# Kernel tuning notes

Hardware: AMD Instinct MI355X
Metric: run time of the kernel (lower is better)

Reference implementation:

```python
import jax, jax.numpy as jnp
import numpy as np

GRAPH_ALPHA = 3.0
HOP_ALPHA = 0.05
TOP_K = 30


def conv1x1(x, W, b):
    # x: [B,C,N,T], W: [O,C] -> [B,O,N,T]
    return jnp.einsum('bcnt,oc->bont', x, W) + b[None, :, None, None]


def tconv(x, W, b):
    # temporal conv along T, kernel (1,3), 'same' padding. W: [O,I,1,3]
    y = jax.lax.conv_general_dilated(x, W, (1, 1), ((0, 0), (1, 1)),
                                     dimension_numbers=('NCHW', 'OIHW', 'NCHW'))
    return y + b[None, :, None, None]


def mixprop(x, adj, W, b):
    # 1-hop mix-prop graph diffusion (gcn_depth=1, hopalpha=0.05)
    n = adj.shape[0]
    A = adj + jnp.eye(n, dtype=adj.dtype)
    A = A / A.sum(axis=1, keepdims=True)
    h = HOP_ALPHA * x + (1.0 - HOP_ALPHA) * jnp.einsum('bcvt,vw->bcwt', x, A)
    return conv1x1(jnp.concatenate([x, h], axis=1), W, b)


def st_block(x, adj, tf_w, tf_b, tg_w, tg_b, g1_w, g1_b, g2_w, g2_b,
             end_w, end_b, out_w, out_b):
    h = jnp.tanh(tconv(x, tf_w, tf_b)) * jax.nn.sigmoid(tconv(x, tg_w, tg_b))
    h = mixprop(h, adj, g1_w, g1_b) + mixprop(h, adj.T, g2_w, g2_b)
    h = jax.nn.relu(conv1x1(h, end_w, end_b))
    return conv1x1(h, out_w, out_b)


def build_adj(idx, emb1, emb2, l1_w, l1_b, l2_w, l2_b):
    e1, e2 = emb1[idx], emb2[idx]
    n1 = jnp.tanh(GRAPH_ALPHA * (e1 @ l1_w.T + l1_b))
    n2 = jnp.tanh(GRAPH_ALPHA * (e2 @ l2_w.T + l2_b))
    a = n1 @ n2.T - n2 @ n1.T
    adj = jax.nn.relu(jnp.tanh(GRAPH_ALPHA * a))
    _, top_idx = jax.lax.top_k(adj, TOP_K)
    rows = jnp.arange(adj.shape[0])[:, None]
    mask = jnp.zeros_like(adj).at[rows, top_idx].set(1.0)
    return adj * mask


def setup_inputs() -> dict:
    B, T, N, D = 16, 128, 1024, 64
    ks = jax.random.split(jax.random.key(0), 24)
    def w(i, shape):
        return jax.random.normal(ks[i], shape, dtype=jnp.float32) * 0.1
    z = lambda *s: jnp.zeros(s, jnp.float32)
    return {
        'x': jax.random.normal(ks[0], (B, T, N), dtype=jnp.float32),
        'idx': jnp.arange(N, dtype=jnp.int32),
        'emb1': w(1, (N, D)), 'emb2': w(2, (N, D)),
        'lin1_w': w(3, (D, D)), 'lin1_b': z(D),
        'lin2_w': w(4, (D, D)), 'lin2_b': z(D),
        'w_start': w(5, (16, 1)), 'b_start': z(16),
        'enc_tf_w': w(6, (16, 16, 1, 3)), 'enc_tf_b': z(16),
        'enc_tg_w': w(7, (16, 16, 1, 3)), 'enc_tg_b': z(16),
        'enc_g1_w': w(8, (16, 32)), 'enc_g1_b': z(16),
        'enc_g2_w': w(9, (16, 32)), 'enc_g2_b': z(16),
        'enc_end_w': w(10, (32, 16)), 'enc_end_b': z(32),
        'enc_out_w': w(11, (64, 32)), 'enc_out_b': z(64),
        'dec_tf_w': w(12, (64, 64, 1, 3)), 'dec_tf_b': z(64),
        'dec_tg_w': w(13, (64, 64, 1, 3)), 'dec_tg_b': z(64),
        'dec_g1_w': w(14, (64, 128)), 'dec_g1_b': z(64),
        'dec_g2_w': w(15, (64, 128)), 'dec_g2_b': z(64),
        'dec_end_w': w(16, (32, 64)), 'dec_end_b': z(32),
        'dec_out_w': w(17, (16, 32)), 'dec_out_b': z(16),
        'w_end': w(18, (1, 16)), 'b_end': z(1),
    }


def reference(x, idx, emb1, emb2, lin1_w, lin1_b, lin2_w, lin2_b,
              w_start, b_start,
              enc_tf_w, enc_tf_b, enc_tg_w, enc_tg_b, enc_g1_w, enc_g1_b,
              enc_g2_w, enc_g2_b, enc_end_w, enc_end_b, enc_out_w, enc_out_b,
              dec_tf_w, dec_tf_b, dec_tg_w, dec_tg_b, dec_g1_w, dec_g1_b,
              dec_g2_w, dec_g2_b, dec_end_w, dec_end_b, dec_out_w, dec_out_b,
              w_end, b_end):
    adj = build_adj(idx, emb1, emb2, lin1_w, lin1_b, lin2_w, lin2_b)
    h = jnp.transpose(x, (0, 2, 1))[:, None]  # [B,1,N,T]
    h = conv1x1(h, w_start, b_start)          # [B,16,N,T]
    z = st_block(h, adj, enc_tf_w, enc_tf_b, enc_tg_w, enc_tg_b,
                 enc_g1_w, enc_g1_b, enc_g2_w, enc_g2_b,
                 enc_end_w, enc_end_b, enc_out_w, enc_out_b)  # [B,64,N,T]
    y = st_block(z, adj, dec_tf_w, dec_tf_b, dec_tg_w, dec_tg_b,
                 dec_g1_w, dec_g1_b, dec_g2_w, dec_g2_b,
                 dec_end_w, dec_end_b, dec_out_w, dec_out_b)  # [B,16,N,T]
    y = conv1x1(y, w_end, b_end)               # [B,1,N,T]
    return jnp.transpose(y[:, 0], (0, 2, 1))   # [B,T,N]
```

## Files before the change

kernel.cpp:

```cpp
#include <hip/hip_runtime.h>
#include <math.h>

#define NN   1024
#define TTL  128
#define NTP  131072
#define TOPK 30

#define OEGTF_T 0
#define OEGTF_C 48
#define OEGTF_B 96
#define OEGTG_T 112
#define OEGTG_C 160
#define OEGTG_B 208
#define OEE0    224
#define OEE1    736
#define OEE2    1248
#define OEEB    1760
#define OEOUT_W 1792
#define OEOUT_B 3840
#define ODTF_B  16192
#define ODTG_B  28544
#define ODEB    34752
#define OWC     34784
#define OBC     34816
#define ODEALL  59456
#define ODTW2   65600
#define OCF     77888
#define OCG     78080
#define WTOT    78272


__global__ void k_prep_weights(
    const float* __restrict__ w_start, const float* __restrict__ b_start,
    const float* __restrict__ etf_w, const float* __restrict__ etf_b,
    const float* __restrict__ etg_w, const float* __restrict__ etg_b,
    const float* __restrict__ eg1_w, const float* __restrict__ eg1_b,
    const float* __restrict__ eg2_w, const float* __restrict__ eg2_b,
    const float* __restrict__ eend_w, const float* __restrict__ eend_b,
    const float* __restrict__ eout_w, const float* __restrict__ eout_b,
    const float* __restrict__ dtf_w, const float* __restrict__ dtf_b,
    const float* __restrict__ dtg_w, const float* __restrict__ dtg_b,
    const float* __restrict__ dg1_w, const float* __restrict__ dg1_b,
    const float* __restrict__ dg2_w, const float* __restrict__ dg2_b,
    const float* __restrict__ dend_w, const float* __restrict__ dend_b,
    const float* __restrict__ dout_w, const float* __restrict__ dout_b,
    const float* __restrict__ w_end, const float* __restrict__ b_end,
    float* __restrict__ W)
{
    int tid = blockIdx.x*blockDim.x + threadIdx.x;
    int nthr = gridDim.x*blockDim.x;
    for (int id=tid; id<96; id+=nthr){
        int which = id/48; int r = id%48; int o = r/3, k = r%3;
        const float* w = which ? etg_w : etf_w;
        double t=0.0, c=0.0;
        for (int i=0;i<16;i++){
            double wv = (double)w[(o*16+i)*3+k];
            t += wv*(double)w_start[i];
            c += wv*(double)b_start[i];
        }
        W[(which?OEGTG_T:OEGTF_T)+o*3+k] = (float)t;
        W[(which?OEGTG_C:OEGTF_C)+o*3+k] = (float)c;
    }
    for (int i=tid;i<16;i+=nthr){
        W[OEGTF_B+i] = etf_b[i];
        W[OEGTG_B+i] = etg_b[i];
    }
    for (int id=tid; id<512; id+=nthr){
        int i = id>>5, o2 = id&31;
        double s0=0.0, s1=0.0, s2=0.0;
        for (int o=0;o<16;o++){
            double m0 = (double)eg1_w[o*32+i] + (double)eg2_w[o*32+i]
                      + 0.05*((double)eg1_w[o*32+16+i] + (double)eg2_w[o*32+16+i]);
            double m1 = 0.95*(double)eg1_w[o*32+16+i];
            double m2 = 0.95*(double)eg2_w[o*32+16+i];
            double ew = (double)eend_w[o2*16+o];
            s0 += ew*m0; s1 += ew*m1; s2 += ew*m2;
        }
        W[OEE0+i*32+o2]=(float)s0; W[OEE1+i*32+o2]=(float)s1; W[OEE2+i*32+o2]=(float)s2;
    }
    for (int o2=tid; o2<32; o2+=nthr){
        double s = (double)eend_b[o2];
        for (int o=0;o<16;o++) s += (double)eend_w[o2*16+o]*((double)eg1_b[o]+(double)eg2_b[o]);
        W[OEEB+o2] = (float)s;
    }
    for (int i=tid;i<64;i+=nthr){
        W[ODTF_B+i]=dtf_b[i]; W[ODTG_B+i]=dtg_b[i];
    }
    for (int id=tid; id<12288; id+=nthr){
        int oc = id/3072; int rem = id%3072; int j = rem/96; int q = rem%96;
        const float* w = (q<48) ? dtf_w : dtg_w;
        int q2 = (q<48) ? q : q-48;
        int o = q2/3, k = q2%3;
        double s = 0.0;
        for (int i=0;i<64;i++)
            s += (double)w[((oc*16+o)*64+i)*3+k]*(double)eout_w[i*32+j];
        W[ODTW2+id] = (float)s;
    }
    for (int id=tid; id<384; id+=nthr){
        int which = id/192; int r = id%192;
        int oc = r/48; int q = r%48; int o = q/3, k = q%3;
        const float* w = which ? dtg_w : dtf_w;
        double s = 0.0;
        for (int i=0;i<64;i++)
            s += (double)w[((oc*16+o)*64+i)*3+k]*(double)eout_b[i];
        W[(which?OCG:OCF) + oc*48 + o*3 + k] = (float)s;
    }
    for (int id=tid; id<6144; id+=nthr){
        int i = id/96, j = id%96;
        double s = 0.0;
        if (j < 32){
            int o2 = j;
            for (int o=0;o<64;o++){
                double m1 = 0.95*(double)dg1_w[o*128+64+i];
                s += (double)dend_w[o2*64+o]*m1;
            }
        } else if (j < 64){
            int o2 = j-32;
            for (int o=0;o<64;o++){
                double m2 = 0.95*(double)dg2_w[o*128+64+i];
                s += (double)dend_w[o2*64+o]*m2;
            }
        } else {
            int o2 = j-64;
            for (int o=0;o<64;o++){
                double m0 = (double)dg1_w[o*128+i] + (double)dg2_w[o*128+i]
                          + 0.05*((double)dg1_w[o*128+64+i] + (double)dg2_w[o*128+64+i]);
                s += (double)dend_w[o2*64+o]*m0;
            }
        }
        W[ODEALL+id] = (float)s;
    }
    for (int o2=tid; o2<32; o2+=nthr){
        double s = (double)dend_b[o2];
        for (int o=0;o<64;o++) s += (double)dend_w[o2*64+o]*((double)dg1_b[o]+(double)dg2_b[o]);
        W[ODEB+o2] = (float)s;
        double wc = 0.0;
        for (int o3=0;o3<16;o3++) wc += (double)w_end[o3]*(double)dout_w[o3*32+o2];
        W[OWC+o2] = (float)wc;
    }
    if (tid==0){
        double bc = (double)b_end[0];
        for (int o3=0;o3<16;o3++) bc += (double)w_end[o3]*(double)dout_b[o3];
        W[OBC] = (float)bc;
    }
}

__global__ void k_emb(const int* __restrict__ idxp,
                      const float* __restrict__ emb1, const float* __restrict__ emb2,
                      const float* __restrict__ l1w, const float* __restrict__ l1b,
                      const float* __restrict__ l2w, const float* __restrict__ l2b,
                      double* __restrict__ n1, double* __restrict__ n2)
{
    int id = blockIdx.x*blockDim.x + threadIdx.x;
    int i = id>>6, d = id&63;
    int ii = idxp[i];
    double a1 = (double)l1b[d], a2 = (double)l2b[d];
    for (int k=0;k<64;k++){
        a1 += (double)emb1[ii*64+k]*(double)l1w[d*64+k];
        a2 += (double)emb2[ii*64+k]*(double)l2w[d*64+k];
    }
    n1[id] = tanh(3.0*a1);
    n2[id] = tanh(3.0*a2);
}

__global__ __launch_bounds__(64) void k_topk(
    const double* __restrict__ n1, const double* __restrict__ n2,
    int* __restrict__ topc, double* __restrict__ topv,
    double* __restrict__ rs1, double* __restrict__ colsum)
{
    __shared__ double arow[NN];
    __shared__ double sn1[64], sn2[64];
    int i = blockIdx.x, lane = threadIdx.x;
    sn1[lane] = n1[i*64+lane];
    sn2[lane] = n2[i*64+lane];
    __syncthreads();
    for (int jb=0;jb<16;jb++){
        int j = jb*64 + lane;
        const double* p2 = n2 + j*64;
        const double* p1 = n1 + j*64;
        double d1v=0.0, d2v=0.0;
        for (int d=0;d<64;d++){ d1v += sn1[d]*p2[d]; d2v += sn2[d]*p1[d]; }
        double a = tanh(3.0*(d1v - d2v));
        arow[j] = a>0.0 ? a : 0.0;
    }
    __syncthreads();
    double rsum = 0.0;
    for (int r=0;r<TOPK;r++){
        double bv = -2.0; int bj = 1<<30;
        for (int jb=0;jb<16;jb++){
            int j = jb*64+lane;
            double v = arow[j];
            if (v>bv || (v==bv && j<bj)){ bv=v; bj=j; }
        }
        for (int off=32; off>=1; off>>=1){
            double ov = __shfl_xor(bv, off, 64);
            int    oj = __shfl_xor(bj, off, 64);
            if (ov>bv || (ov==bv && oj<bj)){ bv=ov; bj=oj; }
        }
        if (lane == (bj & 63)) arow[bj] = -2.0;
        if (lane == 0){
            topc[i*TOPK+r] = bj;
            topv[i*TOPK+r] = bv;
            if (bv > 0.0) atomicAdd(&colsum[bj], bv);
        }
        rsum += (bv > 0.0 ? bv : 0.0);
        __syncthreads();
    }
    if (lane == 0) rs1[i] = 1.0 + rsum;
}

__global__ void k_csc(const int* __restrict__ topc, const double* __restrict__ topv,
                      const double* __restrict__ rs1,
                      int* __restrict__ ccount, int* __restrict__ cidx, float* __restrict__ cw)
{
    int w = blockIdx.x*blockDim.x + threadIdx.x;
    if (w >= NN) return;
    double rv = rs1[w];
    for (int r=0;r<TOPK;r++){
        double v = topv[w*TOPK+r];
        if (v > 0.0){
            int col = topc[w*TOPK+r];
            int pos = atomicAdd(&ccount[col], 1);
            cidx[(long)col*NN+pos] = w;
            cw  [(long)col*NN+pos] = (float)(v / rv);
        }
    }
}

__global__ void k_pad(int* __restrict__ ccount, int* __restrict__ cidx, float* __restrict__ cw)
{
    int col = blockIdx.x*blockDim.x + threadIdx.x;
    if (col >= NN) return;
    int cnt = ccount[col];
    int padded = (cnt + 7) & ~7;
    for (int e = cnt; e < padded; e++){
        cidx[(long)col*NN + e] = 0;
        cw  [(long)col*NN + e] = 0.0f;
    }
    ccount[col] = padded;
}

__global__ void k_post1(const double* __restrict__ colsum, const double* __restrict__ rs1,
                        double* __restrict__ rs2, float* __restrict__ d1, float* __restrict__ d2)
{
    int v = blockIdx.x*blockDim.x + threadIdx.x;
    if (v >= NN) return;
    double r2 = 1.0 + colsum[v];
    rs2[v] = r2;
    d2[v] = (float)(1.0/r2);
    d1[v] = (float)(1.0/rs1[v]);
}

__global__ void k_post2(const int* __restrict__ topc, const double* __restrict__ topv,
                        const double* __restrict__ rs2,
                        int* __restrict__ topc2, float* __restrict__ ew2b)
{
    int e = blockIdx.x*blockDim.x + threadIdx.x;
    if (e >= NN*32) return;
    int w = e>>5, r = e&31;
    if (r < TOPK){
        double v = topv[w*TOPK+r];
        int c = topc[w*TOPK+r];
        topc2[e] = (v > 0.0) ? c : 0;
        ew2b[e]  = (v > 0.0) ? (float)(v / rs2[c]) : 0.0f;
    } else {
        topc2[e] = 0;
        ew2b[e]  = 0.0f;
    }
}


__global__ __launch_bounds__(256) void k_enc_gg(const float* __restrict__ x,
    float* __restrict__ eg, float* __restrict__ es1, float* __restrict__ es2,
    const float* __restrict__ Wt,
    const int* __restrict__ ccount, const int* __restrict__ cidx, const float* __restrict__ cw,
    const int* __restrict__ topc2, const float* __restrict__ ew2b,
    const float* __restrict__ d1, const float* __restrict__ d2,
    long S, int b0)
{
    __shared__ float4 lds4[NN];
    int tid = threadIdx.x, c = blockIdx.y, cb = blockIdx.z, t0 = blockIdx.x*4;
    float ft[3], fc[3], gt[3], gcc[3];
    #pragma unroll
    for (int k=0;k<3;k++){
        ft[k]=Wt[OEGTF_T+c*3+k]; fc[k]=Wt[OEGTF_C+c*3+k];
        gt[k]=Wt[OEGTG_T+c*3+k]; gcc[k]=Wt[OEGTG_C+c*3+k];
    }
    float fb = Wt[OEGTF_B+c], gb = Wt[OEGTG_B+c];
    const float* xb = x + (long)(b0+cb)*NTP + (long)t0*NN;
    long base = (long)c*S + (long)cb*NTP + (long)t0*NN;
    bool hl0 = (t0>0), hr3 = (t0+4<TTL);
    for (int q=0;q<4;q++){
        int v = q*256 + tid;
        float xm = hl0 ? xb[v-NN] : 0.0f;
        float x0 = xb[v], x1 = xb[v+NN], x2 = xb[v+2*NN], x3 = xb[v+3*NN];
        float xq = hr3 ? xb[v+4*NN] : 0.0f;
        float g0,g1,g2,g3;
        {
            float atf = fb + ft[1]*x0 + fc[1], atg = gb + gt[1]*x0 + gcc[1];
            if (hl0){ atf += ft[0]*xm + fc[0]; atg += gt[0]*xm + gcc[0]; }
            atf += ft[2]*x1 + fc[2]; atg += gt[2]*x1 + gcc[2];
            g0 = tanhf(atf)/(1.0f+expf(-atg));
        }
        {
            float atf = fb + ft[0]*x0 + fc[0] + ft[1]*x1 + fc[1] + ft[2]*x2 + fc[2];
            float atg = gb + gt[0]*x0 + gcc[0] + gt[1]*x1 + gcc[1] + gt[2]*x2 + gcc[2];
            g1 = tanhf(atf)/(1.0f+expf(-atg));
        }
        {
            float atf = fb + ft[0]*x1 + fc[0] + ft[1]*x2 + fc[1] + ft[2]*x3 + fc[2];
            float atg = gb + gt[0]*x1 + gcc[0] + gt[1]*x2 + gcc[1] + gt[2]*x3 + gcc[2];
            g2 = tanhf(atf)/(1.0f+expf(-atg));
        }
        {
            float atf = fb + ft[0]*x2 + fc[0] + ft[1]*x3 + fc[1];
            float atg = gb + gt[0]*x2 + gcc[0] + gt[1]*x3 + gcc[1];
            if (hr3){ atf += ft[2]*xq + fc[2]; atg += gt[2]*xq + gcc[2]; }
            g3 = tanhf(atf)/(1.0f+expf(-atg));
        }
        lds4[v] = make_float4(g0,g1,g2,g3);
        eg[base+v] = g0; eg[base+NN+v] = g1; eg[base+2*NN+v] = g2; eg[base+3*NN+v] = g3;
    }
    __syncthreads();
    for (int wb=0;wb<4;wb++){
        int w = wb*256 + tid;
        float4 gw = lds4[w];
        float dv = d1[w];
        float a0=gw.x*dv, a1=gw.y*dv, a2=gw.z*dv, a3=gw.w*dv;
        int cnt = ccount[w];
        const int4*   ci4 = (const int4*)  (cidx + (long)w*NN);
        const float4* cw4 = (const float4*)(cw   + (long)w*NN);
        for (int e=0; e<cnt; e+=8){
            int4 ia = ci4[e>>2], ib = ci4[(e>>2)+1];
            float4 wa = cw4[e>>2], wc = cw4[(e>>2)+1];
            float4 s;
            s = lds4[ia.x]; a0 += wa.x*s.x; a1 += wa.x*s.y; a2 += wa.x*s.z; a3 += wa.x*s.w;
            s = lds4[ia.y]; a0 += wa.y*s.x; a1 += wa.y*s.y; a2 += wa.y*s.z; a3 += wa.y*s.w;
            s = lds4[ia.z]; a0 += wa.z*s.x; a1 += wa.z*s.y; a2 += wa.z*s.z; a3 += wa.z*s.w;
            s = lds4[ia.w]; a0 += wa.w*s.x; a1 += wa.w*s.y; a2 += wa.w*s.z; a3 += wa.w*s.w;
            s = lds4[ib.x]; a0 += wc.x*s.x; a1 += wc.x*s.y; a2 += wc.x*s.z; a3 += wc.x*s.w;
            s = lds4[ib.y]; a0 += wc.y*s.x; a1 += wc.y*s.y; a2 += wc.y*s.z; a3 += wc.y*s.w;
            s = lds4[ib.z]; a0 += wc.z*s.x; a1 += wc.z*s.y; a2 += wc.z*s.z; a3 += wc.z*s.w;
            s = lds4[ib.w]; a0 += wc.w*s.x; a1 += wc.w*s.y; a2 += wc.w*s.z; a3 += wc.w*s.w;
        }
        es1[base+w]=a0; es1[base+NN+w]=a1; es1[base+2*NN+w]=a2; es1[base+3*NN+w]=a3;
        float dw = d2[w];
        float b0a=gw.x*dw, b1a=gw.y*dw, b2a=gw.z*dw, b3a=gw.w*dw;
        const int4*   tc4 = (const int4*)  (topc2 + w*32);
        const float4* e24 = (const float4*)(ew2b  + w*32);
        #pragma unroll
        for (int r=0;r<8;r++){
            int4 ic = tc4[r]; float4 wv = e24[r];
            float4 s;
            s = lds4[ic.x]; b0a += wv.x*s.x; b1a += wv.x*s.y; b2a += wv.x*s.z; b3a += wv.x*s.w;
            s = lds4[ic.y]; b0a += wv.y*s.x; b1a += wv.y*s.y; b2a += wv.y*s.z; b3a += wv.y*s.w;
            s = lds4[ic.z]; b0a += wv.z*s.x; b1a += wv.z*s.y; b2a += wv.z*s.z; b3a += wv.z*s.w;
            s = lds4[ic.w]; b0a += wv.w*s.x; b1a += wv.w*s.y; b2a += wv.w*s.z; b3a += wv.w*s.w;
        }
        es2[base+w]=b0a; es2[base+NN+w]=b1a; es2[base+2*NN+w]=b2a; es2[base+3*NN+w]=b3a;
    }
}

__global__ __launch_bounds__(256) void k_enc_tail(const float* __restrict__ Bp,
    float* __restrict__ E32, const float* __restrict__ Wt, long S)
{
    long p = (long)blockIdx.x*256 + threadIdx.x;
    float e[32];
    #pragma unroll
    for (int o2=0;o2<32;o2++) e[o2] = Wt[OEEB+o2];
    for (int i=0;i<16;i++){
        float a = Bp[(long)i*S+p], b = Bp[(long)(16+i)*S+p], c = Bp[(long)(32+i)*S+p];
        const float* w0 = Wt+OEE0+i*32;
        const float* w1 = Wt+OEE1+i*32;
        const float* w2 = Wt+OEE2+i*32;
        #pragma unroll
        for (int o2=0;o2<32;o2++) e[o2] += w0[o2]*a + w1[o2]*b + w2[o2]*c;
    }
    #pragma unroll
    for (int o2=0;o2<32;o2++){
        float v = e[o2];
        E32[(long)o2*S+p] = v>0.0f ? v : 0.0f;
    }
}

__global__ __launch_bounds__(256) void k_dec_gate(const float* __restrict__ E32,
    float* __restrict__ g, const float* __restrict__ Wt, long S)
{
    int oc = blockIdx.y;
    long pos = (long)blockIdx.x*256 + threadIdx.x;
    int t = (int)((pos>>10) & (TTL-1));
    bool hasL = (t>0), hasR = (t<TTL-1);
    float af[16], ag[16];
    #pragma unroll
    for (int o=0;o<16;o++){
        float bf = Wt[ODTF_B+oc*16+o] + Wt[OCF+oc*48+o*3+1];
        float bg = Wt[ODTG_B+oc*16+o] + Wt[OCG+oc*48+o*3+1];
        if (hasL){ bf += Wt[OCF+oc*48+o*3];   bg += Wt[OCG+oc*48+o*3]; }
        if (hasR){ bf += Wt[OCF+oc*48+o*3+2]; bg += Wt[OCG+oc*48+o*3+2]; }
        af[o]=bf; ag[o]=bg;
    }
    #pragma unroll 1
    for (int j=0;j<32;j++){
        const float* xp = E32 + (long)j*S + pos;
        float xc = xp[0];
        float xl = hasL ? xp[-NN] : 0.0f;
        float xr = hasR ? xp[NN]  : 0.0f;
        const float* wfg = Wt + ODTW2 + (long)(oc*32+j)*96;
        #pragma unroll
        for (int o=0;o<16;o++){
            af[o] += wfg[o*3]*xl + wfg[o*3+1]*xc + wfg[o*3+2]*xr;
            ag[o] += wfg[48+o*3]*xl + wfg[48+o*3+1]*xc + wfg[48+o*3+2]*xr;
        }
    }
    #pragma unroll
    for (int o=0;o<16;o++){
        g[(long)(oc*16+o)*S + pos] = tanhf(af[o])/(1.0f+expf(-ag[o]));
    }
}

__global__ __launch_bounds__(256) void k_dec_conv(const float* __restrict__ g,
    float* __restrict__ Cp, float* __restrict__ P0p,
    const float* __restrict__ Wt, long S)
{
    long p = (long)blockIdx.x*256 + threadIdx.x;
    int jc = blockIdx.y;
    if (jc == 0){
        float a1[32], a2[32];
        #pragma unroll
        for (int jj=0;jj<32;jj++){ a1[jj]=0.0f; a2[jj]=0.0f; }
        #pragma unroll 1
        for (int i=0;i<64;i++){
            float gv = g[(long)i*S+p];
            const float* wr = Wt + ODEALL + i*96;
            #pragma unroll
            for (int jj=0;jj<32;jj++){ a1[jj] += wr[jj]*gv; a2[jj] += wr[32+jj]*gv; }
        }
        #pragma unroll
        for (int jj=0;jj<32;jj++){
            Cp[(long)jj*S+p] = a1[jj];
            Cp[(long)(32+jj)*S+p] = a2[jj];
        }
    } else {
        float a0[32];
        #pragma unroll
        for (int jj=0;jj<32;jj++) a0[jj] = Wt[ODEB+jj];
        #pragma unroll 1
        for (int i=0;i<64;i++){
            float gv = g[(long)i*S+p];
            const float* wr = Wt + ODEALL + i*96 + 64;
            #pragma unroll
            for (int jj=0;jj<32;jj++) a0[jj] += wr[jj]*gv;
        }
        #pragma unroll
        for (int jj=0;jj<32;jj++) P0p[(long)jj*S+p] = a0[jj];
    }
}

__global__ __launch_bounds__(256) void k_graph32(const float* __restrict__ P1,
    const float* __restrict__ P2, float* __restrict__ Q12,
    const int* __restrict__ ccount, const int* __restrict__ cidx, const float* __restrict__ cw,
    const int* __restrict__ topc2, const float* __restrict__ ew2b,
    const float* __restrict__ d1, const float* __restrict__ d2, long S)
{
    __shared__ float4 lds4[2*NN];
    int tid = threadIdx.x;
    int ch = blockIdx.y, cb = blockIdx.z, t0 = blockIdx.x*4;
    long base = (long)ch*S + (long)cb*NTP + (long)t0*NN;
    const float* s1 = P1 + base;
    const float* s2 = P2 + base;
    for (int q=0;q<4;q++){
        int v = q*256 + tid;
        lds4[v]    = make_float4(s1[v], s1[v+NN], s1[v+2*NN], s1[v+3*NN]);
        lds4[NN+v] = make_float4(s2[v], s2[v+NN], s2[v+2*NN], s2[v+3*NN]);
    }
    __syncthreads();
    for (int wb=0;wb<4;wb++){
        int w = wb*256 + tid;
        float4 g1v = lds4[w];
        float dv = d1[w];
        float a0=g1v.x*dv, a1=g1v.y*dv, a2=g1v.z*dv, a3=g1v.w*dv;
        int cnt = ccount[w];
        const int4*   ci4 = (const int4*)  (cidx + (long)w*NN);
        const float4* cw4 = (const float4*)(cw   + (long)w*NN);
        for (int e=0; e<cnt; e+=8){
            int4 ia = ci4[e>>2], ib = ci4[(e>>2)+1];
            float4 wa = cw4[e>>2], wc = cw4[(e>>2)+1];
            float4 s;
            s = lds4[ia.x]; a0 += wa.x*s.x; a1 += wa.x*s.y; a2 += wa.x*s.z; a3 += wa.x*s.w;
            s = lds4[ia.y]; a0 += wa.y*s.x; a1 += wa.y*s.y; a2 += wa.y*s.z; a3 += wa.y*s.w;
            s = lds4[ia.z]; a0 += wa.z*s.x; a1 += wa.z*s.y; a2 += wa.z*s.z; a3 += wa.z*s.w;
            s = lds4[ia.w]; a0 += wa.w*s.x; a1 += wa.w*s.y; a2 += wa.w*s.z; a3 += wa.w*s.w;
            s = lds4[ib.x]; a0 += wc.x*s.x; a1 += wc.x*s.y; a2 += wc.x*s.z; a3 += wc.x*s.w;
            s = lds4[ib.y]; a0 += wc.y*s.x; a1 += wc.y*s.y; a2 += wc.y*s.z; a3 += wc.y*s.w;
            s = lds4[ib.z]; a0 += wc.z*s.x; a1 += wc.z*s.y; a2 += wc.z*s.z; a3 += wc.z*s.w;
            s = lds4[ib.w]; a0 += wc.w*s.x; a1 += wc.w*s.y; a2 += wc.w*s.z; a3 += wc.w*s.w;
        }
        float4 g2v = lds4[NN+w];
        float dw = d2[w];
        float c0=g2v.x*dw, c1=g2v.y*dw, c2=g2v.z*dw, c3=g2v.w*dw;
        const int4*   tc4 = (const int4*)  (topc2 + w*32);
        const float4* e24 = (const float4*)(ew2b  + w*32);
        #pragma unroll
        for (int r=0;r<8;r++){
            int4 ic = tc4[r]; float4 wv = e24[r];
            float4 s;
            s = lds4[NN+ic.x]; c0 += wv.x*s.x; c1 += wv.x*s.y; c2 += wv.x*s.z; c3 += wv.x*s.w;
            s = lds4[NN+ic.y]; c0 += wv.y*s.x; c1 += wv.y*s.y; c2 += wv.y*s.z; c3 += wv.y*s.w;
            s = lds4[NN+ic.z]; c0 += wv.z*s.x; c1 += wv.z*s.y; c2 += wv.z*s.z; c3 += wv.z*s.w;
            s = lds4[NN+ic.w]; c0 += wv.w*s.x; c1 += wv.w*s.y; c2 += wv.w*s.z; c3 += wv.w*s.w;
        }
        Q12[base+w]      = a0+c0;
        Q12[base+NN+w]   = a1+c1;
        Q12[base+2*NN+w] = a2+c2;
        Q12[base+3*NN+w] = a3+c3;
    }
}

__global__ __launch_bounds__(256) void k_dec_tail(const float* __restrict__ P0,
    const float* __restrict__ Q12,
    const float* __restrict__ Wt, float* __restrict__ out, long S, int b0)
{
    long p = (long)blockIdx.x*256 + threadIdx.x;
    float res = Wt[OBC];
    #pragma unroll 8
    for (int o2=0;o2<32;o2++){
        float e = P0[(long)o2*S+p] + Q12[(long)o2*S+p];
        e = e>0.0f ? e : 0.0f;
        res += Wt[OWC+o2]*e;
    }
    out[(long)b0*NTP + p] = res;
}


extern "C" void kernel_launch(void* const* d_in, const int* in_sizes, int n_in,
                              void* d_out, int out_size, void* d_ws, size_t ws_size,
                              hipStream_t stream)
{
    const float* x      = (const float*)d_in[0];
    const int*   idx    = (const int*)  d_in[1];
    const float* emb1   = (const float*)d_in[2];
    const float* emb2   = (const float*)d_in[3];
    const float* lin1_w = (const float*)d_in[4];
    const float* lin1_b = (const float*)d_in[5];
    const float* lin2_w = (const float*)d_in[6];
    const float* lin2_b = (const float*)d_in[7];
    const float* w_start= (const float*)d_in[8];
    const float* b_start= (const float*)d_in[9];
    const float* etf_w  = (const float*)d_in[10];
    const float* etf_b  = (const float*)d_in[11];
    const float* etg_w  = (const float*)d_in[12];
    const float* etg_b  = (const float*)d_in[13];
    const float* eg1_w  = (const float*)d_in[14];
    const float* eg1_b  = (const float*)d_in[15];
    const float* eg2_w  = (const float*)d_in[16];
    const float* eg2_b  = (const float*)d_in[17];
    const float* eend_w = (const float*)d_in[18];
    const float* eend_b = (const float*)d_in[19];
    const float* eout_w = (const float*)d_in[20];
    const float* eout_b = (const float*)d_in[21];
    const float* dtf_w  = (const float*)d_in[22];
    const float* dtf_b  = (const float*)d_in[23];
    const float* dtg_w  = (const float*)d_in[24];
    const float* dtg_b  = (const float*)d_in[25];
    const float* dg1_w  = (const float*)d_in[26];
    const float* dg1_b  = (const float*)d_in[27];
    const float* dg2_w  = (const float*)d_in[28];
    const float* dg2_b  = (const float*)d_in[29];
    const float* dend_w = (const float*)d_in[30];
    const float* dend_b = (const float*)d_in[31];
    const float* dout_w = (const float*)d_in[32];
    const float* dout_b = (const float*)d_in[33];
    const float* w_end  = (const float*)d_in[34];
    const float* b_end  = (const float*)d_in[35];
    float* out = (float*)d_out;

    char* basep = (char*)d_ws;
    size_t cur = 0;
    auto alloc = [&](size_t bytes)->void* {
        void* p = basep + cur;
        cur = (cur + bytes + 511) & ~(size_t)511;
        return p;
    };
    float*  W     = (float*) alloc(WTOT*sizeof(float));
    double* n1    = (double*)alloc(65536*sizeof(double));
    double* n2    = (double*)alloc(65536*sizeof(double));
    double* topv  = (double*)alloc((size_t)NN*TOPK*sizeof(double));
    int*    topc  = (int*)   alloc((size_t)NN*TOPK*sizeof(int));
    double* rs1   = (double*)alloc(NN*sizeof(double));
    double* rs2   = (double*)alloc(NN*sizeof(double));
    double* colsum= (double*)alloc(NN*sizeof(double));
    float*  d1a   = (float*) alloc(NN*sizeof(float));
    float*  d2a   = (float*) alloc(NN*sizeof(float));
    int*    topc2 = (int*)   alloc((size_t)NN*32*sizeof(int));
    float*  ew2b  = (float*) alloc((size_t)NN*32*sizeof(float));
    int*    ccount= (int*)   alloc(NN*sizeof(int));
    int*    cidx  = (int*)   alloc((size_t)NN*NN*sizeof(int));
    float*  cw    = (float*) alloc((size_t)NN*NN*sizeof(float));

    size_t perb = (size_t)176 * NTP * sizeof(float);
    int CB = 1;
    for (int c = 16; c >= 1; c >>= 1){
        if (cur + perb*(size_t)c <= ws_size){ CB = c; break; }
    }
    long S = (long)CB * NTP;
    float* A = (float*)alloc((size_t)64*S*sizeof(float));
    float* B = (float*)alloc((size_t)48*S*sizeof(float));
    float* C = (float*)alloc((size_t)64*S*sizeof(float));

    (void)hipMemsetAsync(colsum, 0, NN*sizeof(double), stream);
    (void)hipMemsetAsync(ccount, 0, NN*sizeof(int), stream);

    k_prep_weights<<<32,256,0,stream>>>(
        w_start,b_start, etf_w,etf_b, etg_w,etg_b, eg1_w,eg1_b, eg2_w,eg2_b,
        eend_w,eend_b, eout_w,eout_b, dtf_w,dtf_b, dtg_w,dtg_b, dg1_w,dg1_b,
        dg2_w,dg2_b, dend_w,dend_b, dout_w,dout_b, w_end,b_end, W);
    k_emb<<<256,256,0,stream>>>(idx, emb1, emb2, lin1_w, lin1_b, lin2_w, lin2_b, n1, n2);
    k_topk<<<NN,64,0,stream>>>(n1, n2, topc, topv, rs1, colsum);
    k_csc<<<4,256,0,stream>>>(topc, topv, rs1, ccount, cidx, cw);
    k_pad<<<4,256,0,stream>>>(ccount, cidx, cw);
    k_post1<<<4,256,0,stream>>>(colsum, rs1, rs2, d1a, d2a);
    k_post2<<<(NN*32+255)/256,256,0,stream>>>(topc, topv, rs2, topc2, ew2b);

    int nch = 16 / CB;
    for (int ch=0; ch<nch; ch++){
        int b0 = ch*CB;
        k_enc_gg<<<dim3(32,16,CB),256,0,stream>>>(x, B, B+(long)16*S, B+(long)32*S, W,
            ccount,cidx,cw, topc2,ew2b, d1a,d2a, S, b0);
        k_enc_tail<<<512*CB,256,0,stream>>>(B, A, W, S);
        k_dec_gate<<<dim3(512*CB,4),256,0,stream>>>(A, C, W, S);
        k_dec_conv<<<dim3(512*CB,2),256,0,stream>>>(C, A, B, W, S);
        k_graph32<<<dim3(32,32,CB),256,0,stream>>>(A, A+(long)32*S, C,
            ccount,cidx,cw, topc2,ew2b, d1a,d2a, S);
        k_dec_tail<<<512*CB,256,0,stream>>>(B, C, W, out, S, b0);
    }
    (void)in_sizes; (void)n_in; (void)out_size;
}
```

Measured before the change: 3.764 ms.

## Fuse decoder graph, tail and end conv; compute two timesteps per gate thread

Widens the top-k kernel to 256 threads with a cross-wave reduction, so the dot-product and selection work is spread over more lanes. The decoder gate now computes two adjacent timesteps per thread, sharing the loaded input taps and weights. The two halves of the decoder 1x1 conv are merged into one pass over g. The graph-diffusion kernel now also applies the residual add, ReLU and final end-weight reduction over groups of 4 channels and writes 8 partial sums, which a small combine kernel adds up. This avoids writing and rereading the Q12 intermediate, at the cost of higher register pressure and less parallelism per launch.

```diff
diff --git a/kernel.cpp b/kernel.cpp
--- a/kernel.cpp
+++ b/kernel.cpp
@@ -163,21 +163,23 @@
     n2[id] = tanh(3.0*a2);
 }
 
-__global__ __launch_bounds__(64) void k_topk(
+__global__ __launch_bounds__(256) void k_topk(
     const double* __restrict__ n1, const double* __restrict__ n2,
     int* __restrict__ topc, double* __restrict__ topv,
     double* __restrict__ rs1, double* __restrict__ colsum)
 {
     __shared__ double arow[NN];
     __shared__ double sn1[64], sn2[64];
-    int i = blockIdx.x, lane = threadIdx.x;
-    sn1[lane] = n1[i*64+lane];
-    sn2[lane] = n2[i*64+lane];
+    __shared__ double rvs[4];
+    __shared__ int    rjs[4];
+    int i = blockIdx.x, tid = threadIdx.x;
+    int lane = tid & 63, wid = tid >> 6;
+    if (tid < 64){ sn1[tid] = n1[i*64+tid]; sn2[tid] = n2[i*64+tid]; }
     __syncthreads();
-    for (int jb=0;jb<16;jb++){
-        int j = jb*64 + lane;
-        const double* p2 = n2 + j*64;
-        const double* p1 = n1 + j*64;
+    for (int jb=0;jb<4;jb++){
+        int j = jb*256 + tid;
+        const double* p2 = n2 + (long)j*64;
+        const double* p1 = n1 + (long)j*64;
         double d1v=0.0, d2v=0.0;
         for (int d=0;d<64;d++){ d1v += sn1[d]*p2[d]; d2v += sn2[d]*p1[d]; }
         double a = tanh(3.0*(d1v - d2v));
@@ -187,8 +189,9 @@
     double rsum = 0.0;
     for (int r=0;r<TOPK;r++){
         double bv = -2.0; int bj = 1<<30;
-        for (int jb=0;jb<16;jb++){
-            int j = jb*64+lane;
+        #pragma unroll
+        for (int jb=0;jb<4;jb++){
+            int j = jb*256+tid;
             double v = arow[j];
             if (v>bv || (v==bv && j<bj)){ bv=v; bj=j; }
         }
@@ -197,8 +200,16 @@
             int    oj = __shfl_xor(bj, off, 64);
             if (ov>bv || (ov==bv && oj<bj)){ bv=ov; bj=oj; }
         }
-        if (lane == (bj & 63)) arow[bj] = -2.0;
-        if (lane == 0){
+        if (lane == 0){ rvs[wid]=bv; rjs[wid]=bj; }
+        __syncthreads();
+        bv = rvs[0]; bj = rjs[0];
+        #pragma unroll
+        for (int k2=1;k2<4;k2++){
+            double ov = rvs[k2]; int oj = rjs[k2];
+            if (ov>bv || (ov==bv && oj<bj)){ bv=ov; bj=oj; }
+        }
+        if (tid == (bj & 255)) arow[bj] = -2.0;
+        if (tid == 0){
             topc[i*TOPK+r] = bj;
             topv[i*TOPK+r] = bv;
             if (bv > 0.0) atomicAdd(&colsum[bj], bv);
@@ -206,7 +217,7 @@
         rsum += (bv > 0.0 ? bv : 0.0);
         __syncthreads();
     }
-    if (lane == 0) rs1[i] = 1.0 + rsum;
+    if (tid == 0) rs1[i] = 1.0 + rsum;
 }
 
 __global__ void k_csc(const int* __restrict__ topc, const double* __restrict__ topv,
@@ -386,149 +397,183 @@
 __global__ __launch_bounds__(256) void k_dec_gate(const float* __restrict__ E32,
     float* __restrict__ g, const float* __restrict__ Wt, long S)
 {
-    int oc = blockIdx.y;
-    long pos = (long)blockIdx.x*256 + threadIdx.x;
-    int t = (int)((pos>>10) & (TTL-1));
-    bool hasL = (t>0), hasR = (t<TTL-1);
-    float af[16], ag[16];
+    int oc = blockIdx.y, cb = blockIdx.z;
+    int bx = blockIdx.x;
+    int vseg = bx & 3, tpair = bx >> 2;
+    int t0 = tpair*2;
+    long pos0 = (long)cb*NTP + (long)t0*NN + vseg*256 + threadIdx.x;
+    bool hasL = (t0 > 0), hasR = (t0 + 2 < TTL);
+    float af0[16], ag0[16], af1[16], ag1[16];
+    const float* CFo = Wt + OCF + oc*48;
+    const float* CGo = Wt + OCG + oc*48;
     #pragma unroll
     for (int o=0;o<16;o++){
-        float bf = Wt[ODTF_B+oc*16+o] + Wt[OCF+oc*48+o*3+1];
-        float bg = Wt[ODTG_B+oc*16+o] + Wt[OCG+oc*48+o*3+1];
-        if (hasL){ bf += Wt[OCF+oc*48+o*3];   bg += Wt[OCG+oc*48+o*3]; }
-        if (hasR){ bf += Wt[OCF+oc*48+o*3+2]; bg += Wt[OCG+oc*48+o*3+2]; }
-        af[o]=bf; ag[o]=bg;
-    }
-    #pragma unroll 1
+        float fB = Wt[ODTF_B+oc*16+o], gB = Wt[ODTG_B+oc*16+o];
+        float f0 = CFo[o*3], f1 = CFo[o*3+1], f2 = CFo[o*3+2];
+        float h0 = CGo[o*3], h1 = CGo[o*3+1], h2 = CGo[o*3+2];
+        af0[o] = fB + f1 + f2 + (hasL ? f0 : 0.0f);
+        ag0[o] = gB + h1 + h2 + (hasL ? h0 : 0.0f);
+        af1[o] = fB + f0 + f1 + (hasR ? f2 : 0.0f);
+        ag1[o] = gB + h0 + h1 + (hasR ? h2 : 0.0f);
+    }
+    #pragma unroll 2
     for (int j=0;j<32;j++){
-        const float* xp = E32 + (long)j*S + pos;
-        float xc = xp[0];
-        float xl = hasL ? xp[-NN] : 0.0f;
-        float xr = hasR ? xp[NN]  : 0.0f;
+        const float* xp = E32 + (long)j*S + pos0;
+        float xl0 = hasL ? xp[-NN] : 0.0f;
+        float xc0 = xp[0];
+        float xc1 = xp[NN];
+        float xr1 = hasR ? xp[2*NN] : 0.0f;
         const float* wfg = Wt + ODTW2 + (long)(oc*32+j)*96;
         #pragma unroll
         for (int o=0;o<16;o++){
-            af[o] += wfg[o*3]*xl + wfg[o*3+1]*xc + wfg[o*3+2]*xr;
-            ag[o] += wfg[48+o*3]*xl + wfg[48+o*3+1]*xc + wfg[48+o*3+2]*xr;
+            float w0=wfg[o*3], w1=wfg[o*3+1], w2=wfg[o*3+2];
+            af0[o] += w0*xl0 + w1*xc0 + w2*xc1;
+            af1[o] += w0*xc0 + w1*xc1 + w2*xr1;
+            float v0=wfg[48+o*3], v1=wfg[48+o*3+1], v2=wfg[48+o*3+2];
+            ag0[o] += v0*xl0 + v1*xc0 + v2*xc1;
+            ag1[o] += v0*xc0 + v1*xc1 + v2*xr1;
         }
     }
     #pragma unroll
     for (int o=0;o<16;o++){
-        g[(long)(oc*16+o)*S + pos] = tanhf(af[o])/(1.0f+expf(-ag[o]));
+        long op = (long)(oc*16+o)*S + pos0;
+        g[op]    = tanhf(af0[o])/(1.0f+expf(-ag0[o]));
+        g[op+NN] = tanhf(af1[o])/(1.0f+expf(-ag1[o]));
     }
 }
 
 __global__ __launch_bounds__(256) void k_dec_conv(const float* __restrict__ g,
-    float* __restrict__ Cp, float* __restrict__ P0p,
+    float* __restrict__ P12, float* __restrict__ P0p,
     const float* __restrict__ Wt, long S)
 {
     long p = (long)blockIdx.x*256 + threadIdx.x;
-    int jc = blockIdx.y;
-    if (jc == 0){
-        float a1[32], a2[32];
-        #pragma unroll
-        for (int jj=0;jj<32;jj++){ a1[jj]=0.0f; a2[jj]=0.0f; }
-        #pragma unroll 1
-        for (int i=0;i<64;i++){
-            float gv = g[(long)i*S+p];
-            const float* wr = Wt + ODEALL + i*96;
-            #pragma unroll
-            for (int jj=0;jj<32;jj++){ a1[jj] += wr[jj]*gv; a2[jj] += wr[32+jj]*gv; }
-        }
+    float a0[32], a1[32], a2[32];
+    #pragma unroll
+    for (int jj=0;jj<32;jj++){ a1[jj]=0.0f; a2[jj]=0.0f; a0[jj]=Wt[ODEB+jj]; }
+    #pragma unroll 1
+    for (int i=0;i<64;i++){
+        float gv = g[(long)i*S+p];
+        const float* wr = Wt + ODEALL + i*96;
         #pragma unroll
         for (int jj=0;jj<32;jj++){
-            Cp[(long)jj*S+p] = a1[jj];
-            Cp[(long)(32+jj)*S+p] = a2[jj];
-        }
-    } else {
-        float a0[32];
-        #pragma unroll
-        for (int jj=0;jj<32;jj++) a0[jj] = Wt[ODEB+jj];
-        #pragma unroll 1
-        for (int i=0;i<64;i++){
-            float gv = g[(long)i*S+p];
-            const float* wr = Wt + ODEALL + i*96 + 64;
-            #pragma unroll
-            for (int jj=0;jj<32;jj++) a0[jj] += wr[jj]*gv;
-        }
-        #pragma unroll
-        for (int jj=0;jj<32;jj++) P0p[(long)jj*S+p] = a0[jj];
-    }
-}
-
-__global__ __launch_bounds__(256) void k_graph32(const float* __restrict__ P1,
-    const float* __restrict__ P2, float* __restrict__ Q12,
+            a1[jj] += wr[jj]*gv;
+            a2[jj] += wr[32+jj]*gv;
+            a0[jj] += wr[64+jj]*gv;
+        }
+    }
+    #pragma unroll
+    for (int jj=0;jj<32;jj++){
+        P12[(long)jj*S+p]      = a1[jj];
+        P12[(long)(32+jj)*S+p] = a2[jj];
+        P0p[(long)jj*S+p]      = a0[jj];
+    }
+}
+
+__global__ __launch_bounds__(256) void k_graph32f(const float* __restrict__ P1,
+    const float* __restrict__ P2, const float* __restrict__ P0,
+    float* __restrict__ part,
     const int* __restrict__ ccount, const int* __restrict__ cidx, const float* __restrict__ cw,
     const int* __restrict__ topc2, const float* __restrict__ ew2b,
-    const float* __restrict__ d1, const float* __restrict__ d2, long S)
-{
-    __shared__ float4 lds4[2*NN];
+    const float* __restrict__ d1, const float* __restrict__ d2,
+    const float* __restrict__ Wt, long S)
+{
+    __shared__ float4 lds4[NN];
     int tid = threadIdx.x;
-    int ch = blockIdx.y, cb = blockIdx.z, t0 = blockIdx.x*4;
-    long base = (long)ch*S + (long)cb*NTP + (long)t0*NN;
-    const float* s1 = P1 + base;
-    const float* s2 = P2 + base;
-    for (int q=0;q<4;q++){
-        int v = q*256 + tid;
-        lds4[v]    = make_float4(s1[v], s1[v+NN], s1[v+2*NN], s1[v+3*NN]);
-        lds4[NN+v] = make_float4(s2[v], s2[v+NN], s2[v+2*NN], s2[v+3*NN]);
-    }
-    __syncthreads();
+    int grp = blockIdx.y, cb = blockIdx.z, t0 = blockIdx.x*4;
+    long tbase = (long)cb*NTP + (long)t0*NN;
+    float res[4][4];
+    #pragma unroll
+    for (int wb=0;wb<4;wb++){
+        #pragma unroll
+        for (int k=0;k<4;k++) res[wb][k]=0.0f;
+    }
+    float q1[4][4];
+    for (int c4=0;c4<4;c4++){
+        int ch = grp*4 + c4;
+        long base = (long)ch*S + tbase;
+        if (c4) __syncthreads();
+        const float* s1 = P1 + base;
+        for (int q=0;q<4;q++){
+            int v = q*256 + tid;
+            lds4[v] = make_float4(s1[v], s1[v+NN], s1[v+2*NN], s1[v+3*NN]);
+        }
+        __syncthreads();
+        for (int wb=0;wb<4;wb++){
+            int w = wb*256 + tid;
+            float4 gv = lds4[w];
+            float dv = d1[w];
+            float a0=gv.x*dv, a1=gv.y*dv, a2=gv.z*dv, a3=gv.w*dv;
+            int cnt = ccount[w];
+            const int4*   ci4 = (const int4*)  (cidx + (long)w*NN);
+            const float4* cw4 = (const float4*)(cw   + (long)w*NN);
+            for (int e=0; e<cnt; e+=8){
+                int4 ia = ci4[e>>2], ib = ci4[(e>>2)+1];
+                float4 wa = cw4[e>>2], wc2 = cw4[(e>>2)+1];
+                float4 s;
+                s = lds4[ia.x]; a0 += wa.x*s.x; a1 += wa.x*s.y; a2 += wa.x*s.z; a3 += wa.x*s.w;
+                s = lds4[ia.y]; a0 += wa.y*s.x; a1 += wa.y*s.y; a2 += wa.y*s.z; a3 += wa.y*s.w;
+                s = lds4[ia.z]; a0 += wa.z*s.x; a1 += wa.z*s.y; a2 += wa.z*s.z; a3 += wa.z*s.w;
+                s = lds4[ia.w]; a0 += wa.w*s.x; a1 += wa.w*s.y; a2 += wa.w*s.z; a3 += wa.w*s.w;
+                s = lds4[ib.x]; a0 += wc2.x*s.x; a1 += wc2.x*s.y; a2 += wc2.x*s.z; a3 += wc2.x*s.w;
+                s = lds4[ib.y]; a0 += wc2.y*s.x; a1 += wc2.y*s.y; a2 += wc2.y*s.z; a3 += wc2.y*s.w;
+                s = lds4[ib.z]; a0 += wc2.z*s.x; a1 += wc2.z*s.y; a2 += wc2.z*s.z; a3 += wc2.z*s.w;
+                s = lds4[ib.w]; a0 += wc2.w*s.x; a1 += wc2.w*s.y; a2 += wc2.w*s.z; a3 += wc2.w*s.w;
+            }
+            q1[wb][0]=a0; q1[wb][1]=a1; q1[wb][2]=a2; q1[wb][3]=a3;
+        }
+        __syncthreads();
+        const float* s2 = P2 + base;
+        for (int q=0;q<4;q++){
+            int v = q*256 + tid;
+            lds4[v] = make_float4(s2[v], s2[v+NN], s2[v+2*NN], s2[v+3*NN]);
+        }
+        __syncthreads();
+        float wc = Wt[OWC+ch];
+        const float* p0 = P0 + base;
+        for (int wb=0;wb<4;wb++){
+            int w = wb*256 + tid;
+            float4 gv = lds4[w];
+            float dw = d2[w];
+            float c0=gv.x*dw, c1=gv.y*dw, c2=gv.z*dw, c3=gv.w*dw;
+            const int4*   tc4 = (const int4*)  (topc2 + w*32);
+            const float4* e24 = (const float4*)(ew2b  + w*32);
+            #pragma unroll
+            for (int r=0;r<8;r++){
+                int4 ic = tc4[r]; float4 wv = e24[r];
+                float4 s;
+                s = lds4[ic.x]; c0 += wv.x*s.x; c1 += wv.x*s.y; c2 += wv.x*s.z; c3 += wv.x*s.w;
+                s = lds4[ic.y]; c0 += wv.y*s.x; c1 += wv.y*s.y; c2 += wv.y*s.z; c3 += wv.y*s.w;
+                s = lds4[ic.z]; c0 += wv.z*s.x; c1 += wv.z*s.y; c2 += wv.z*s.z; c3 += wv.z*s.w;
+                s = lds4[ic.w]; c0 += wv.w*s.x; c1 += wv.w*s.y; c2 += wv.w*s.z; c3 += wv.w*s.w;
+            }
+            float e0 = p0[w]        + q1[wb][0] + c0;
+            float e1 = p0[NN+w]     + q1[wb][1] + c1;
+            float e2 = p0[2*NN+w]   + q1[wb][2] + c2;
+            float e3 = p0[3*NN+w]   + q1[wb][3] + c3;
+            e0 = e0>0.0f?e0:0.0f; e1 = e1>0.0f?e1:0.0f;
+            e2 = e2>0.0f?e2:0.0f; e3 = e3>0.0f?e3:0.0f;
+            res[wb][0] += wc*e0; res[wb][1] += wc*e1;
+            res[wb][2] += wc*e2; res[wb][3] += wc*e3;
+        }
+    }
+    long pb = (long)grp*S + tbase;
     for (int wb=0;wb<4;wb++){
         int w = wb*256 + tid;
-        float4 g1v = lds4[w];
-        float dv = d1[w];
-        float a0=g1v.x*dv, a1=g1v.y*dv, a2=g1v.z*dv, a3=g1v.w*dv;
-        int cnt = ccount[w];
-        const int4*   ci4 = (const int4*)  (cidx + (long)w*NN);
-        const float4* cw4 = (const float4*)(cw   + (long)w*NN);
-        for (int e=0; e<cnt; e+=8){
-            int4 ia = ci4[e>>2], ib = ci4[(e>>2)+1];
-            float4 wa = cw4[e>>2], wc = cw4[(e>>2)+1];
-            float4 s;
-            s = lds4[ia.x]; a0 += wa.x*s.x; a1 += wa.x*s.y; a2 += wa.x*s.z; a3 += wa.x*s.w;
-            s = lds4[ia.y]; a0 += wa.y*s.x; a1 += wa.y*s.y; a2 += wa.y*s.z; a3 += wa.y*s.w;
-            s = lds4[ia.z]; a0 += wa.z*s.x; a1 += wa.z*s.y; a2 += wa.z*s.z; a3 += wa.z*s.w;
-            s = lds4[ia.w]; a0 += wa.w*s.x; a1 += wa.w*s.y; a2 += wa.w*s.z; a3 += wa.w*s.w;
-            s = lds4[ib.x]; a0 += wc.x*s.x; a1 += wc.x*s.y; a2 += wc.x*s.z; a3 += wc.x*s.w;
-            s = lds4[ib.y]; a0 += wc.y*s.x; a1 += wc.y*s.y; a2 += wc.y*s.z; a3 += wc.y*s.w;
-            s = lds4[ib.z]; a0 += wc.z*s.x; a1 += wc.z*s.y; a2 += wc.z*s.z; a3 += wc.z*s.w;
-            s = lds4[ib.w]; a0 += wc.w*s.x; a1 += wc.w*s.y; a2 += wc.w*s.z; a3 += wc.w*s.w;
-        }
-        float4 g2v = lds4[NN+w];
-        float dw = d2[w];
-        float c0=g2v.x*dw, c1=g2v.y*dw, c2=g2v.z*dw, c3=g2v.w*dw;
-        const int4*   tc4 = (const int4*)  (topc2 + w*32);
-        const float4* e24 = (const float4*)(ew2b  + w*32);
-        #pragma unroll
-        for (int r=0;r<8;r++){
-            int4 ic = tc4[r]; float4 wv = e24[r];
-            float4 s;
-            s = lds4[NN+ic.x]; c0 += wv.x*s.x; c1 += wv.x*s.y; c2 += wv.x*s.z; c3 += wv.x*s.w;
-            s = lds4[NN+ic.y]; c0 += wv.y*s.x; c1 += wv.y*s.y; c2 += wv.y*s.z; c3 += wv.y*s.w;
-            s = lds4[NN+ic.z]; c0 += wv.z*s.x; c1 += wv.z*s.y; c2 += wv.z*s.z; c3 += wv.z*s.w;
-            s = lds4[NN+ic.w]; c0 += wv.w*s.x; c1 += wv.w*s.y; c2 += wv.w*s.z; c3 += wv.w*s.w;
-        }
-        Q12[base+w]      = a0+c0;
-        Q12[base+NN+w]   = a1+c1;
-        Q12[base+2*NN+w] = a2+c2;
-        Q12[base+3*NN+w] = a3+c3;
-    }
-}
-
-__global__ __launch_bounds__(256) void k_dec_tail(const float* __restrict__ P0,
-    const float* __restrict__ Q12,
+        part[pb+w]      = res[wb][0];
+        part[pb+NN+w]   = res[wb][1];
+        part[pb+2*NN+w] = res[wb][2];
+        part[pb+3*NN+w] = res[wb][3];
+    }
+}
+
+__global__ __launch_bounds__(256) void k_comb(const float* __restrict__ part,
     const float* __restrict__ Wt, float* __restrict__ out, long S, int b0)
 {
     long p = (long)blockIdx.x*256 + threadIdx.x;
-    float res = Wt[OBC];
-    #pragma unroll 8
-    for (int o2=0;o2<32;o2++){
-        float e = P0[(long)o2*S+p] + Q12[(long)o2*S+p];
-        e = e>0.0f ? e : 0.0f;
-        res += Wt[OWC+o2]*e;
-    }
-    out[(long)b0*NTP + p] = res;
+    float r = Wt[OBC];
+    #pragma unroll
+    for (int gp=0; gp<8; gp++) r += part[(long)gp*S+p];
+    out[(long)b0*NTP + p] = r;
 }
 
 
@@ -615,7 +660,7 @@
         eend_w,eend_b, eout_w,eout_b, dtf_w,dtf_b, dtg_w,dtg_b, dg1_w,dg1_b,
         dg2_w,dg2_b, dend_w,dend_b, dout_w,dout_b, w_end,b_end, W);
     k_emb<<<256,256,0,stream>>>(idx, emb1, emb2, lin1_w, lin1_b, lin2_w, lin2_b, n1, n2);
-    k_topk<<<NN,64,0,stream>>>(n1, n2, topc, topv, rs1, colsum);
+    k_topk<<<NN,256,0,stream>>>(n1, n2, topc, topv, rs1, colsum);
     k_csc<<<4,256,0,stream>>>(topc, topv, rs1, ccount, cidx, cw);
     k_pad<<<4,256,0,stream>>>(ccount, cidx, cw);
     k_post1<<<4,256,0,stream>>>(colsum, rs1, rs2, d1a, d2a);
@@ -627,11 +672,11 @@
         k_enc_gg<<<dim3(32,16,CB),256,0,stream>>>(x, B, B+(long)16*S, B+(long)32*S, W,
             ccount,cidx,cw, topc2,ew2b, d1a,d2a, S, b0);
         k_enc_tail<<<512*CB,256,0,stream>>>(B, A, W, S);
-        k_dec_gate<<<dim3(512*CB,4),256,0,stream>>>(A, C, W, S);
-        k_dec_conv<<<dim3(512*CB,2),256,0,stream>>>(C, A, B, W, S);
-        k_graph32<<<dim3(32,32,CB),256,0,stream>>>(A, A+(long)32*S, C,
-            ccount,cidx,cw, topc2,ew2b, d1a,d2a, S);
-        k_dec_tail<<<512*CB,256,0,stream>>>(B, C, W, out, S, b0);
+        k_dec_gate<<<dim3(256,4,CB),256,0,stream>>>(A, C, W, S);
+        k_dec_conv<<<512*CB,256,0,stream>>>(C, A, B, W, S);
+        k_graph32f<<<dim3(32,8,CB),256,0,stream>>>(A, A+(long)32*S, B, C,
+            ccount,cidx,cw, topc2,ew2b, d1a,d2a, W, S);
+        k_comb<<<512*CB,256,0,stream>>>(C, W, out, S, b0);
     }
     (void)in_sizes; (void)n_in; (void)out_size;
 }
```

Result: slower. 4.010 ms (+6.5%).
